# Performance work log

Hardware: AMD Instinct MI355X
Metric: run time of the kernel (lower is better)

## Reference

```python
import jax, jax.numpy as jnp
import numpy as np

B, S, D, H = 4, 2048, 1024, 16
HD = D // H  # head_dim = 64


def setup_inputs() -> dict:
    key = jax.random.key(0)
    ks = jax.random.split(key, 5)
    scale = 0.02
    return {
        "x": jax.random.normal(ks[0], (B, S, D), dtype=jnp.float32),
        "Wq": jax.random.normal(ks[1], (D, D), dtype=jnp.float32) * scale,
        "Wk": jax.random.normal(ks[2], (D, D), dtype=jnp.float32) * scale,
        "Wv": jax.random.normal(ks[3], (D, D), dtype=jnp.float32) * scale,
        "Wo": jax.random.normal(ks[4], (D, D), dtype=jnp.float32) * scale,
        "bo": jnp.zeros((D,), dtype=jnp.float32),
    }


def reference(x, Wq, Wk, Wv, Wo, bo):
    b, s, d = x.shape
    # projections (no bias on q/k/v, matching qkv_bias=False)
    q = (x @ Wq).reshape(b, s, H, HD).transpose(0, 2, 1, 3)  # [B,H,S,HD]
    k = (x @ Wk).reshape(b, s, H, HD).transpose(0, 2, 1, 3)
    v = (x @ Wv).reshape(b, s, H, HD).transpose(0, 2, 1, 3)
    scores = jnp.einsum("bhqd,bhkd->bhqk", q, k) / jnp.sqrt(jnp.float32(HD))
    causal = jnp.tril(jnp.ones((s, s), dtype=bool))  # True = keep
    scores = jnp.where(causal, scores, -jnp.inf)
    attn = jax.nn.softmax(scores, axis=-1)
    # dropout p=0.0 -> identity
    out = jnp.einsum("bhqk,bhkd->bhqd", attn, v)
    out = out.transpose(0, 2, 1, 3).reshape(b, s, d)
    return out @ Wo + bo
```

## Files before the change

### kernel.cpp

```cpp
#include <hip/hip_runtime.h>

typedef unsigned short u16;
typedef unsigned int u32;
typedef __attribute__((ext_vector_type(4))) float f32x4;
typedef __attribute__((ext_vector_type(8))) __bf16 bf16x8;
typedef __attribute__((ext_vector_type(4))) _Float16 f16x4;
typedef __attribute__((ext_vector_type(4))) u16 u16x4;
typedef __attribute__((ext_vector_type(4))) u32 u32x4;
typedef __attribute__((ext_vector_type(2))) u32 u32x2;

#define D_ 1024
#define S_ 2048
#define B_ 4
#define H_ 16
#define HD_ 64
#define M_ 8192
#define LDP 72
#define QSCALE 0.18033688011112042591f

__device__ __forceinline__ u16 f2bf(float f) {
  u32 u = __float_as_uint(f);
  u += 0x7fffu + ((u >> 16) & 1u);
  return (u16)(u >> 16);
}

__device__ __forceinline__ float max3f(float a, float b, float c) {
  return fmaxf(fmaxf(a, b), c);
}

__device__ __forceinline__ void gload_lds16(const void* g, void* l) {
  __builtin_amdgcn_global_load_lds((const __attribute__((address_space(1))) void*)g,
                                   (__attribute__((address_space(3))) void*)l, 16, 0, 0);
}

__global__ __launch_bounds__(256) void prep_kernel(const float* __restrict__ x, u16* __restrict__ xb,
                                                   const float* __restrict__ Wq, const float* __restrict__ Wk,
                                                   const float* __restrict__ Wv, const float* __restrict__ Wo,
                                                   u16* __restrict__ Wqt, u16* __restrict__ Wkt,
                                                   u16* __restrict__ Wvt, u16* __restrict__ Wot) {
  __shared__ float lds[64][65];
  int lin = blockIdx.x;
  if (lin < 8192) {
    int i = (lin * 256 + threadIdx.x) * 4;
    f32x4 v = *(const f32x4*)(x + i);
    u16x4 o = {f2bf(v[0]), f2bf(v[1]), f2bf(v[2]), f2bf(v[3])};
    *(u16x4*)(xb + i) = o;
    return;
  }
  int pos = lin - 8192;
  int z = pos >> 8, rem = pos & 255;
  const float* W = z == 0 ? Wq : z == 1 ? Wk : z == 2 ? Wv : Wo;
  u16* Wt       = z == 0 ? Wqt : z == 1 ? Wkt : z == 2 ? Wvt : Wot;
  int k0 = (rem >> 4) * 64, n0 = (rem & 15) * 64;
  int tr = threadIdx.x >> 6, tc = threadIdx.x & 63;
#pragma unroll
  for (int i = 0; i < 16; ++i)
    lds[tr + i * 4][tc] = W[(size_t)(k0 + tr + i * 4) * D_ + n0 + tc];
  __syncthreads();
#pragma unroll
  for (int i = 0; i < 16; ++i)
    Wt[(size_t)(n0 + tr + i * 4) * D_ + k0 + tc] = f2bf(lds[tc][tr + i * 4]);
}

__device__ __forceinline__ void gemm_main(const u16* __restrict__ A, const u16* __restrict__ Bt,
                                          u16* As, u16* Bs, int row0, int col0, f32x4 acc[4][4]) {
  const int tid = threadIdx.x;
  const int lane = tid & 63, wave = tid >> 6;
  const int wr = wave >> 1, wc = wave & 1;
  const int l15 = lane & 15, lg = lane >> 4;
  const int sr8 = lane >> 3;
  const int scx = (lane & 7) ^ sr8;
#pragma unroll 1
  for (int k0 = 0; k0 < D_; k0 += 64) {
#pragma unroll
    for (int it = 0; it < 4; ++it) {
      int rbase = (it * 4 + wave) * 8;
      int r = rbase + sr8;
      gload_lds16(A + (size_t)(row0 + r) * D_ + k0 + scx * 8, As + rbase * 64);
      gload_lds16(Bt + (size_t)(col0 + r) * D_ + k0 + scx * 8, Bs + rbase * 64);
    }
    __syncthreads();
#pragma unroll
    for (int kk = 0; kk < 64; kk += 32) {
      const int cb = kk >> 3;
      bf16x8 af[4], bf[4];
#pragma unroll
      for (int m = 0; m < 4; ++m) {
        int row = wr * 64 + m * 16 + l15;
        af[m] = *(const bf16x8*)(As + row * 64 + (((cb + lg) ^ (l15 & 7)) << 3));
      }
#pragma unroll
      for (int n = 0; n < 4; ++n) {
        int row = wc * 64 + n * 16 + l15;
        bf[n] = *(const bf16x8*)(Bs + row * 64 + (((cb + lg) ^ (l15 & 7)) << 3));
      }
#pragma unroll
      for (int m = 0; m < 4; ++m)
#pragma unroll
        for (int n = 0; n < 4; ++n)
          acc[m][n] = __builtin_amdgcn_mfma_f32_16x16x32_bf16(af[m], bf[n], acc[m][n], 0, 0, 0);
    }
    __syncthreads();
  }
}

__global__ __launch_bounds__(256) void qkv_gemm_kernel(const u16* __restrict__ xb,
                                                       const u16* __restrict__ Wqt, const u16* __restrict__ Wkt,
                                                       const u16* __restrict__ Wvt,
                                                       u16* __restrict__ Qb, u16* __restrict__ Kb,
                                                       _Float16* __restrict__ Vt) {
  __shared__ u16 As[128 * 64];
  __shared__ u16 Bs[128 * 64];
  int lin = blockIdx.x;
  int xcd = lin & 7, pos = lin >> 3;
  int mode = pos / 64;
  int rem = pos & 63;
  int by = xcd * 8 + (rem >> 3);
  int bx = rem & 7;
  const u16* Bt = mode == 0 ? Wqt : mode == 1 ? Wkt : Wvt;
  f32x4 acc[4][4] = {};
  int row0 = by * 128, col0 = bx * 128;
  gemm_main(xb, Bt, As, Bs, row0, col0, acc);
  int lane = threadIdx.x & 63, wave = threadIdx.x >> 6;
  int wr = wave >> 1, wc = wave & 1, l15 = lane & 15, lg = lane >> 4;
  int rbase = row0 + wr * 64 + lg * 4, cbase = col0 + wc * 64 + l15;
  if (mode == 2) {
#pragma unroll
    for (int m = 0; m < 4; ++m) {
      int row = rbase + m * 16;
      int b = row >> 11, s = row & (S_ - 1);
#pragma unroll
      for (int n = 0; n < 4; ++n) {
        int col = cbase + n * 16;
        int h = col >> 6, hd = col & 63;
        f16x4 vv = {(_Float16)acc[m][n][0], (_Float16)acc[m][n][1],
                    (_Float16)acc[m][n][2], (_Float16)acc[m][n][3]};
        *(f16x4*)(Vt + ((size_t)((b << 4) + h) * HD_ + hd) * S_ + s) = vv;
      }
    }
  } else {
    u16* dst = mode == 0 ? Qb : Kb;
    float scl = mode == 0 ? QSCALE : 1.0f;
#pragma unroll
    for (int m = 0; m < 4; ++m)
#pragma unroll
      for (int n = 0; n < 4; ++n) {
        int col = cbase + n * 16;
#pragma unroll
        for (int r = 0; r < 4; ++r) {
          int row = rbase + m * 16 + r;
          dst[(size_t)row * D_ + col] = f2bf(acc[m][n][r] * scl);
        }
      }
  }
}

__global__ __launch_bounds__(256) void attn_kernel(const u16* __restrict__ Qb, const u16* __restrict__ Kb,
                                                   const _Float16* __restrict__ Vt, u16* __restrict__ attnb) {
  __shared__ u16 Ks[64][LDP];
  __shared__ _Float16 Vs[64][LDP];
  const int tid = threadIdx.x;
  const int wave = tid >> 6, lane = tid & 63;
  const int l15 = lane & 15, lg = lane >> 4;
  const int lin = blockIdx.x;
  const int xcd = lin & 7, slot = lin >> 3;
  const int qblk = 31 - (slot >> 3);
  const int bh = (slot & 7) * 8 + xcd;
  const int b = bh >> 4, h = bh & 15;
  const int ntiles = qblk + 1;
  const int q0 = qblk * 64 + wave * 16;

  const int srow = tid >> 3;
  const int scol = (tid & 7) * 8;
  const u16* Kg = Kb + (size_t)(b * S_) * D_ + h * HD_;
  const _Float16* Vg = Vt + (size_t)bh * HD_ * S_;

  const u16* Qrow = Qb + (size_t)(b * S_ + q0 + l15) * D_ + h * HD_;
  bf16x8 qf0 = *(const bf16x8*)(Qrow + lg * 8);
  bf16x8 qf1 = *(const bf16x8*)(Qrow + 32 + lg * 8);

  float m = -1e30f, lsum = 0.f;
  f32x4 o[4] = {};
  u32x4 kreg0, kreg1, vreg0, vreg1;

  kreg0 = *(const u32x4*)(Kg + (size_t)(srow) * D_ + scol);
  kreg1 = *(const u32x4*)(Kg + (size_t)(32 + srow) * D_ + scol);
  vreg0 = *(const u32x4*)(Vg + (size_t)srow * S_ + scol);
  vreg1 = *(const u32x4*)(Vg + (size_t)(32 + srow) * S_ + scol);

#pragma unroll 1
  for (int t = 0; t < ntiles; ++t) {
    __syncthreads();
    *(u32x4*)(&Ks[srow][scol]) = kreg0;
    *(u32x4*)(&Ks[32 + srow][scol]) = kreg1;
    *(u32x4*)(&Vs[srow][scol]) = vreg0;
    *(u32x4*)(&Vs[32 + srow][scol]) = vreg1;
    __syncthreads();
    if (t + 1 < ntiles) {
      int kv0n = (t + 1) * 64;
      kreg0 = *(const u32x4*)(Kg + (size_t)(kv0n + srow) * D_ + scol);
      kreg1 = *(const u32x4*)(Kg + (size_t)(kv0n + 32 + srow) * D_ + scol);
      vreg0 = *(const u32x4*)(Vg + (size_t)srow * S_ + kv0n + scol);
      vreg1 = *(const u32x4*)(Vg + (size_t)(32 + srow) * S_ + kv0n + scol);
    }
    f32x4 s[4];
    __builtin_amdgcn_s_setprio(1);
#pragma unroll
    for (int j = 0; j < 4; ++j) {
      bf16x8 kf0 = *(const bf16x8*)(&Ks[j * 16 + l15][lg * 8]);
      bf16x8 kf1 = *(const bf16x8*)(&Ks[j * 16 + l15][32 + lg * 8]);
      f32x4 z = {0.f, 0.f, 0.f, 0.f};
      z = __builtin_amdgcn_mfma_f32_16x16x32_bf16(kf0, qf0, z, 0, 0, 0);
      z = __builtin_amdgcn_mfma_f32_16x16x32_bf16(kf1, qf1, z, 0, 0, 0);
      s[j] = z;
    }
    __builtin_amdgcn_s_setprio(0);
    if (t == ntiles - 1) {
      int qr = wave * 16 + l15;
#pragma unroll
      for (int j = 0; j < 4; ++j)
#pragma unroll
        for (int r = 0; r < 4; ++r)
          if (j * 16 + lg * 4 + r > qr) s[j][r] = -1e30f;
    }
    float x0 = max3f(s[0][0], s[0][1], s[0][2]);
    float x1 = max3f(s[0][3], s[1][0], s[1][1]);
    float x2 = max3f(s[1][2], s[1][3], s[2][0]);
    float x3 = max3f(s[2][1], s[2][2], s[2][3]);
    float x4 = max3f(s[3][0], s[3][1], s[3][2]);
    float tmax = fmaxf(max3f(x0, x1, x2), max3f(x3, x4, s[3][3]));
    tmax = fmaxf(tmax, __shfl_xor(tmax, 16));
    tmax = fmaxf(tmax, __shfl_xor(tmax, 32));
    if (!__all(tmax - m <= 8.f)) {
      float nm = fmaxf(m, tmax);
      float alpha = exp2f(m - nm);
      m = nm;
      lsum *= alpha;
#pragma unroll
      for (int hf = 0; hf < 4; ++hf) o[hf] *= alpha;
    }
    f16x4 pb[4];
#pragma unroll
    for (int j = 0; j < 4; ++j) {
      float p0 = exp2f(s[j][0] - m), p1 = exp2f(s[j][1] - m);
      float p2 = exp2f(s[j][2] - m), p3 = exp2f(s[j][3] - m);
      lsum += (p0 + p1) + (p2 + p3);
      u32 lo = __builtin_bit_cast(u32, __builtin_amdgcn_cvt_pkrtz(p0, p1));
      u32 hi = __builtin_bit_cast(u32, __builtin_amdgcn_cvt_pkrtz(p2, p3));
      pb[j] = __builtin_bit_cast(f16x4, (u32x2){lo, hi});
    }
    __builtin_amdgcn_s_setprio(1);
#pragma unroll
    for (int j = 0; j < 4; ++j) {
#pragma unroll
      for (int hf = 0; hf < 4; ++hf) {
        f16x4 vf = *(const f16x4*)(&Vs[hf * 16 + l15][j * 16 + lg * 4]);
        o[hf] = __builtin_amdgcn_mfma_f32_16x16x16f16(vf, pb[j], o[hf], 0, 0, 0);
      }
    }
    __builtin_amdgcn_s_setprio(0);
  }
  lsum += __shfl_xor(lsum, 16);
  lsum += __shfl_xor(lsum, 32);
  float inv = 1.0f / lsum;
  u16* Orow = attnb + (size_t)(b * S_ + q0 + l15) * D_ + h * HD_ + lg * 4;
#pragma unroll
  for (int hf = 0; hf < 4; ++hf) {
    u16x4 ov = {f2bf(o[hf][0] * inv), f2bf(o[hf][1] * inv),
                f2bf(o[hf][2] * inv), f2bf(o[hf][3] * inv)};
    *(u16x4*)(Orow + hf * 16) = ov;
  }
}

__global__ __launch_bounds__(256) void out_gemm_kernel(const u16* __restrict__ attnb, const u16* __restrict__ Wot,
                                                       const float* __restrict__ bo, float* __restrict__ outp) {
  __shared__ u16 As[128 * 64];
  __shared__ u16 Bs[128 * 64];
  int lin = blockIdx.x;
  int xcd = lin & 7, pos = lin >> 3;
  int by = xcd * 8 + (pos >> 3);
  int bx = pos & 7;
  f32x4 acc[4][4] = {};
  int row0 = by * 128, col0 = bx * 128;
  gemm_main(attnb, Wot, As, Bs, row0, col0, acc);
  int lane = threadIdx.x & 63, wave = threadIdx.x >> 6;
  int wr = wave >> 1, wc = wave & 1, l15 = lane & 15, lg = lane >> 4;
  int rbase = row0 + wr * 64 + lg * 4, cbase = col0 + wc * 64 + l15;
#pragma unroll
  for (int n = 0; n < 4; ++n) {
    float bn = bo[cbase + n * 16];
#pragma unroll
    for (int m = 0; m < 4; ++m)
#pragma unroll
      for (int r = 0; r < 4; ++r)
        outp[(size_t)(rbase + m * 16 + r) * D_ + cbase + n * 16] = acc[m][n][r] + bn;
  }
}

extern "C" void kernel_launch(void* const* d_in, const int* in_sizes, int n_in,
                              void* d_out, int out_size, void* d_ws, size_t ws_size,
                              hipStream_t stream) {
  const float* x  = (const float*)d_in[0];
  const float* Wq = (const float*)d_in[1];
  const float* Wk = (const float*)d_in[2];
  const float* Wv = (const float*)d_in[3];
  const float* Wo = (const float*)d_in[4];
  const float* bo = (const float*)d_in[5];
  float* outp = (float*)d_out;

  char* ws = (char*)d_ws;
  u16* xb        = (u16*)(ws);
  u16* Wqt       = (u16*)(ws + ((size_t)16 << 20));
  u16* Wkt       = (u16*)(ws + ((size_t)18 << 20));
  u16* Wvt       = (u16*)(ws + ((size_t)20 << 20));
  u16* Wot       = (u16*)(ws + ((size_t)22 << 20));
  u16* Qb        = (u16*)(ws + ((size_t)24 << 20));
  u16* Kb        = (u16*)(ws + ((size_t)40 << 20));
  _Float16* Vt   = (_Float16*)(ws + ((size_t)56 << 20));
  u16* attnb     = (u16*)(ws + ((size_t)72 << 20));

  prep_kernel<<<dim3(9216), dim3(256), 0, stream>>>(x, xb, Wq, Wk, Wv, Wo, Wqt, Wkt, Wvt, Wot);
  qkv_gemm_kernel<<<dim3(1536), dim3(256), 0, stream>>>(xb, Wqt, Wkt, Wvt, Qb, Kb, Vt);
  attn_kernel<<<dim3(2048), dim3(256), 0, stream>>>(Qb, Kb, Vt, attnb);
  out_gemm_kernel<<<dim3(512), dim3(256), 0, stream>>>(attnb, Wot, bo, outp);
}
```

Baseline: 188.1 us.

## Switch attention to 32x32 MFMA tiles with two waves per block

```diff
diff --git a/kernel.cpp b/kernel.cpp
--- a/kernel.cpp
+++ b/kernel.cpp
@@ -3,8 +3,10 @@
 typedef unsigned short u16;
 typedef unsigned int u32;
 typedef __attribute__((ext_vector_type(4))) float f32x4;
+typedef __attribute__((ext_vector_type(16))) float f32x16;
 typedef __attribute__((ext_vector_type(8))) __bf16 bf16x8;
 typedef __attribute__((ext_vector_type(4))) _Float16 f16x4;
+typedef __attribute__((ext_vector_type(8))) _Float16 f16x8;
 typedef __attribute__((ext_vector_type(4))) u16 u16x4;
 typedef __attribute__((ext_vector_type(4))) u32 u32x4;
 typedef __attribute__((ext_vector_type(2))) u32 u32x2;
@@ -155,121 +157,157 @@
   }
 }
 
-__global__ __launch_bounds__(256) void attn_kernel(const u16* __restrict__ Qb, const u16* __restrict__ Kb,
+__global__ __launch_bounds__(128) void attn_kernel(const u16* __restrict__ Qb, const u16* __restrict__ Kb,
                                                    const _Float16* __restrict__ Vt, u16* __restrict__ attnb) {
   __shared__ u16 Ks[64][LDP];
   __shared__ _Float16 Vs[64][LDP];
   const int tid = threadIdx.x;
   const int wave = tid >> 6, lane = tid & 63;
-  const int l15 = lane & 15, lg = lane >> 4;
+  const int l31 = lane & 31, hi = lane >> 5;
   const int lin = blockIdx.x;
   const int xcd = lin & 7, slot = lin >> 3;
   const int qblk = 31 - (slot >> 3);
   const int bh = (slot & 7) * 8 + xcd;
   const int b = bh >> 4, h = bh & 15;
   const int ntiles = qblk + 1;
-  const int q0 = qblk * 64 + wave * 16;
-
-  const int srow = tid >> 3;
-  const int scol = (tid & 7) * 8;
-  const u16* Kg = Kb + (size_t)(b * S_) * D_ + h * HD_;
-  const _Float16* Vg = Vt + (size_t)bh * HD_ * S_;
-
-  const u16* Qrow = Qb + (size_t)(b * S_ + q0 + l15) * D_ + h * HD_;
-  bf16x8 qf0 = *(const bf16x8*)(Qrow + lg * 8);
-  bf16x8 qf1 = *(const bf16x8*)(Qrow + 32 + lg * 8);
+  const int wq0 = qblk * 64 + wave * 32;
+  const int qg = wq0 + l31;
+
+  const int srow = tid >> 1;
+  const int sh = (tid & 1) * 32;
+  const u16* Kp = Kb + (size_t)(b * S_ + srow) * D_ + h * HD_ + sh;
+  const _Float16* Vp = Vt + ((size_t)bh * HD_ + srow) * S_ + sh;
+
+  const u16* Qrow = Qb + (size_t)(b * S_ + qg) * D_ + h * HD_;
+  bf16x8 qf[4];
+#pragma unroll
+  for (int ds = 0; ds < 4; ++ds)
+    qf[ds] = *(const bf16x8*)(Qrow + ds * 16 + hi * 8);
 
   float m = -1e30f, lsum = 0.f;
-  f32x4 o[4] = {};
-  u32x4 kreg0, kreg1, vreg0, vreg1;
-
-  kreg0 = *(const u32x4*)(Kg + (size_t)(srow) * D_ + scol);
-  kreg1 = *(const u32x4*)(Kg + (size_t)(32 + srow) * D_ + scol);
-  vreg0 = *(const u32x4*)(Vg + (size_t)srow * S_ + scol);
-  vreg1 = *(const u32x4*)(Vg + (size_t)(32 + srow) * S_ + scol);
+  f32x16 oL = {}, oH = {};
+  u32x4 kst[4], vst[4];
+
+#pragma unroll
+  for (int c = 0; c < 4; ++c) {
+    kst[c] = *(const u32x4*)(Kp + c * 8);
+    vst[c] = *(const u32x4*)(Vp + c * 8);
+  }
+  Kp += (size_t)64 * D_;
+  Vp += 64;
 
 #pragma unroll 1
   for (int t = 0; t < ntiles; ++t) {
     __syncthreads();
-    *(u32x4*)(&Ks[srow][scol]) = kreg0;
-    *(u32x4*)(&Ks[32 + srow][scol]) = kreg1;
-    *(u32x4*)(&Vs[srow][scol]) = vreg0;
-    *(u32x4*)(&Vs[32 + srow][scol]) = vreg1;
+#pragma unroll
+    for (int c = 0; c < 4; ++c) {
+      *(u32x4*)(&Ks[srow][sh + c * 8]) = kst[c];
+      *(u32x4*)(&Vs[srow][sh + c * 8]) = vst[c];
+    }
     __syncthreads();
     if (t + 1 < ntiles) {
-      int kv0n = (t + 1) * 64;
-      kreg0 = *(const u32x4*)(Kg + (size_t)(kv0n + srow) * D_ + scol);
-      kreg1 = *(const u32x4*)(Kg + (size_t)(kv0n + 32 + srow) * D_ + scol);
-      vreg0 = *(const u32x4*)(Vg + (size_t)srow * S_ + kv0n + scol);
-      vreg1 = *(const u32x4*)(Vg + (size_t)(32 + srow) * S_ + kv0n + scol);
-    }
-    f32x4 s[4];
+#pragma unroll
+      for (int c = 0; c < 4; ++c) {
+        kst[c] = *(const u32x4*)(Kp + c * 8);
+        vst[c] = *(const u32x4*)(Vp + c * 8);
+      }
+      Kp += (size_t)64 * D_;
+      Vp += 64;
+    }
+    f32x16 sA = {}, sB = {};
     __builtin_amdgcn_s_setprio(1);
 #pragma unroll
-    for (int j = 0; j < 4; ++j) {
-      bf16x8 kf0 = *(const bf16x8*)(&Ks[j * 16 + l15][lg * 8]);
-      bf16x8 kf1 = *(const bf16x8*)(&Ks[j * 16 + l15][32 + lg * 8]);
-      f32x4 z = {0.f, 0.f, 0.f, 0.f};
-      z = __builtin_amdgcn_mfma_f32_16x16x32_bf16(kf0, qf0, z, 0, 0, 0);
-      z = __builtin_amdgcn_mfma_f32_16x16x32_bf16(kf1, qf1, z, 0, 0, 0);
-      s[j] = z;
+    for (int ds = 0; ds < 4; ++ds) {
+      bf16x8 k0 = *(const bf16x8*)(&Ks[l31][ds * 16 + hi * 8]);
+      bf16x8 k1 = *(const bf16x8*)(&Ks[32 + l31][ds * 16 + hi * 8]);
+      sA = __builtin_amdgcn_mfma_f32_32x32x16_bf16(k0, qf[ds], sA, 0, 0, 0);
+      sB = __builtin_amdgcn_mfma_f32_32x32x16_bf16(k1, qf[ds], sB, 0, 0, 0);
     }
     __builtin_amdgcn_s_setprio(0);
     if (t == ntiles - 1) {
-      int qr = wave * 16 + l15;
-#pragma unroll
-      for (int j = 0; j < 4; ++j)
-#pragma unroll
-        for (int r = 0; r < 4; ++r)
-          if (j * 16 + lg * 4 + r > qr) s[j][r] = -1e30f;
-    }
-    float x0 = max3f(s[0][0], s[0][1], s[0][2]);
-    float x1 = max3f(s[0][3], s[1][0], s[1][1]);
-    float x2 = max3f(s[1][2], s[1][3], s[2][0]);
-    float x3 = max3f(s[2][1], s[2][2], s[2][3]);
-    float x4 = max3f(s[3][0], s[3][1], s[3][2]);
-    float tmax = fmaxf(max3f(x0, x1, x2), max3f(x3, x4, s[3][3]));
-    tmax = fmaxf(tmax, __shfl_xor(tmax, 16));
+      const int kvb = t * 64;
+#pragma unroll
+      for (int r = 0; r < 16; ++r) {
+        int off = (r & 3) + 8 * (r >> 2) + 4 * hi;
+        if (kvb + off > qg) sA[r] = -1e30f;
+        if (kvb + 32 + off > qg) sB[r] = -1e30f;
+      }
+    }
+    float mx[16];
+#pragma unroll
+    for (int r = 0; r < 16; ++r) mx[r] = fmaxf(sA[r], sB[r]);
+    float y0 = max3f(mx[0], mx[1], mx[2]);
+    float y1 = max3f(mx[3], mx[4], mx[5]);
+    float y2 = max3f(mx[6], mx[7], mx[8]);
+    float y3 = max3f(mx[9], mx[10], mx[11]);
+    float y4 = max3f(mx[12], mx[13], mx[14]);
+    float tmax = fmaxf(max3f(y0, y1, y2), max3f(y3, y4, mx[15]));
     tmax = fmaxf(tmax, __shfl_xor(tmax, 32));
     if (!__all(tmax - m <= 8.f)) {
       float nm = fmaxf(m, tmax);
       float alpha = exp2f(m - nm);
       m = nm;
       lsum *= alpha;
-#pragma unroll
-      for (int hf = 0; hf < 4; ++hf) o[hf] *= alpha;
-    }
-    f16x4 pb[4];
-#pragma unroll
-    for (int j = 0; j < 4; ++j) {
-      float p0 = exp2f(s[j][0] - m), p1 = exp2f(s[j][1] - m);
-      float p2 = exp2f(s[j][2] - m), p3 = exp2f(s[j][3] - m);
-      lsum += (p0 + p1) + (p2 + p3);
-      u32 lo = __builtin_bit_cast(u32, __builtin_amdgcn_cvt_pkrtz(p0, p1));
-      u32 hi = __builtin_bit_cast(u32, __builtin_amdgcn_cvt_pkrtz(p2, p3));
-      pb[j] = __builtin_bit_cast(f16x4, (u32x2){lo, hi});
+      oL *= alpha;
+      oH *= alpha;
+    }
+    float psum = 0.f;
+#pragma unroll
+    for (int r = 0; r < 16; ++r) {
+      sA[r] = exp2f(sA[r] - m);
+      sB[r] = exp2f(sB[r] - m);
+      psum += sA[r] + sB[r];
+    }
+    lsum += psum;
+    u32 uA[8], uB[8], vA[8], vB[8];
+#pragma unroll
+    for (int k = 0; k < 8; ++k) {
+      uA[k] = __builtin_bit_cast(u32, __builtin_amdgcn_cvt_pkrtz(sA[2 * k], sA[2 * k + 1]));
+      uB[k] = __builtin_bit_cast(u32, __builtin_amdgcn_cvt_pkrtz(sB[2 * k], sB[2 * k + 1]));
+    }
+#pragma unroll
+    for (int k = 0; k < 8; ++k) {
+      vA[k] = __shfl_xor(uA[k], 32);
+      vB[k] = __shfl_xor(uB[k], 32);
     }
     __builtin_amdgcn_s_setprio(1);
 #pragma unroll
-    for (int j = 0; j < 4; ++j) {
-#pragma unroll
-      for (int hf = 0; hf < 4; ++hf) {
-        f16x4 vf = *(const f16x4*)(&Vs[hf * 16 + l15][j * 16 + lg * 4]);
-        o[hf] = __builtin_amdgcn_mfma_f32_16x16x16f16(vf, pb[j], o[hf], 0, 0, 0);
-      }
+    for (int ks = 0; ks < 4; ++ks) {
+      const u32* U = (ks >> 1) ? uB : uA;
+      const u32* Vw = (ks >> 1) ? vB : vA;
+      const int b4 = (ks & 1) * 4;
+      u32 w0 = hi ? Vw[b4 + 2] : U[b4 + 0];
+      u32 w1 = hi ? Vw[b4 + 3] : U[b4 + 1];
+      u32 w2 = hi ? U[b4 + 2] : Vw[b4 + 0];
+      u32 w3 = hi ? U[b4 + 3] : Vw[b4 + 1];
+      f16x8 pa = __builtin_bit_cast(f16x8, (u32x4){w0, w1, w2, w3});
+      f16x8 v0 = *(const f16x8*)(&Vs[l31][ks * 16 + hi * 8]);
+      f16x8 v1 = *(const f16x8*)(&Vs[32 + l31][ks * 16 + hi * 8]);
+      oL = __builtin_amdgcn_mfma_f32_32x32x16_f16(v0, pa, oL, 0, 0, 0);
+      oH = __builtin_amdgcn_mfma_f32_32x32x16_f16(v1, pa, oH, 0, 0, 0);
     }
     __builtin_amdgcn_s_setprio(0);
   }
-  lsum += __shfl_xor(lsum, 16);
+
   lsum += __shfl_xor(lsum, 32);
   float inv = 1.0f / lsum;
-  u16* Orow = attnb + (size_t)(b * S_ + q0 + l15) * D_ + h * HD_ + lg * 4;
-#pragma unroll
-  for (int hf = 0; hf < 4; ++hf) {
-    u16x4 ov = {f2bf(o[hf][0] * inv), f2bf(o[hf][1] * inv),
-                f2bf(o[hf][2] * inv), f2bf(o[hf][3] * inv)};
-    *(u16x4*)(Orow + hf * 16) = ov;
-  }
+  __syncthreads();
+  u16* scr = &Ks[wave * 32 + l31][0];
+#pragma unroll
+  for (int a = 0; a < 4; ++a) {
+    u16x4 pl = {f2bf(oL[4 * a + 0] * inv), f2bf(oL[4 * a + 1] * inv),
+                f2bf(oL[4 * a + 2] * inv), f2bf(oL[4 * a + 3] * inv)};
+    *(u16x4*)(scr + 8 * a + 4 * hi) = pl;
+    u16x4 ph = {f2bf(oH[4 * a + 0] * inv), f2bf(oH[4 * a + 1] * inv),
+                f2bf(oH[4 * a + 2] * inv), f2bf(oH[4 * a + 3] * inv)};
+    *(u16x4*)(scr + 32 + 8 * a + 4 * hi) = ph;
+  }
+  asm volatile("s_waitcnt lgkmcnt(0)" ::: "memory");
+  const u16* srd = &Ks[wave * 32 + l31][hi * 32];
+  u16* Og = attnb + (size_t)(b * S_ + wq0 + l31) * D_ + h * HD_ + hi * 32;
+#pragma unroll
+  for (int c = 0; c < 4; ++c)
+    *(u32x4*)(Og + c * 8) = *(const u32x4*)(srd + c * 8);
 }
 
 __global__ __launch_bounds__(256) void out_gemm_kernel(const u16* __restrict__ attnb, const u16* __restrict__ Wot,
@@ -321,6 +359,6 @@
 
   prep_kernel<<<dim3(9216), dim3(256), 0, stream>>>(x, xb, Wq, Wk, Wv, Wo, Wqt, Wkt, Wvt, Wot);
   qkv_gemm_kernel<<<dim3(1536), dim3(256), 0, stream>>>(xb, Wqt, Wkt, Wvt, Qb, Kb, Vt);
-  attn_kernel<<<dim3(2048), dim3(256), 0, stream>>>(Qb, Kb, Vt, attnb);
+  attn_kernel<<<dim3(2048), dim3(128), 0, stream>>>(Qb, Kb, Vt, attnb);
   out_gemm_kernel<<<dim3(512), dim3(256), 0, stream>>>(attnb, Wot, bo, outp);
 }
```

Result: no change. 187.7 us (-0.2%).
